# Kernel tuning notes

Hardware: AMD Instinct MI355X
Metric: run time of the kernel (lower is better)

Reference implementation:

```python
import jax, jax.numpy as jnp
import numpy as np


def setup_inputs() -> dict:
    key = jax.random.key(0)
    k1, k2 = jax.random.split(key)
    B, Lq, Lc, D = 16, 512, 2048, 1024
    question = jax.random.normal(k1, (B, Lq, D), dtype=jnp.float32)
    context = jax.random.normal(k2, (B, Lc, D), dtype=jnp.float32)
    return {"question": question, "context": context}


def reference(question, context):
    # e = context @ question^T : [B, Lc, Lq]  (unscaled)
    e = jnp.einsum("bcd,bqd->bcq", context, question)
    attn = jax.nn.softmax(e, axis=-1)
    # attention_output = attn @ question : [B, Lc, D]
    attn_out = jnp.einsum("bcq,bqd->bcd", attn, question)
    # concat along feature dim -> [B, Lc, 2D]; dropout is identity at eval
    return jnp.concatenate([context, attn_out], axis=-1)
```

## Files before the change

kernel.cpp:

```cpp
#include <hip/hip_runtime.h>

#define GAS __attribute__((address_space(1)))
#define LAS __attribute__((address_space(3)))

typedef __attribute__((ext_vector_type(8))) _Float16 half8;
typedef __attribute__((ext_vector_type(4))) float floatx4;
typedef __attribute__((ext_vector_type(4))) unsigned short ushort4v;

static constexpr int B_  = 16;
static constexpr int LQ  = 512;
static constexpr int LC  = 2048;
static constexpr int D_  = 1024;
static constexpr int DO  = 2048;
static constexpr int MT  = 64;

__device__ __forceinline__ void gl2lds16(const void* g, void* l) {
  __builtin_amdgcn_global_load_lds((const GAS unsigned int*)g,
                                   (LAS unsigned int*)l, 16, 0, 0);
}

__device__ __forceinline__ unsigned short f2h(float f) {
  return __builtin_bit_cast(unsigned short, (_Float16)f);
}

__global__ void conv_kernel(const float* __restrict__ src,
                            unsigned short* __restrict__ dst, int n4) {
  int i = blockIdx.x * blockDim.x + threadIdx.x;
  const int stride = gridDim.x * blockDim.x;
  for (; i < n4; i += stride) {
    const float4 v = ((const float4*)src)[i];
    ushort4v h;
    h.x = f2h(v.x); h.y = f2h(v.y); h.z = f2h(v.z); h.w = f2h(v.w);
    ((ushort4v*)dst)[i] = h;
  }
}

__global__ void qtransh_kernel(const unsigned short* __restrict__ qh,
                               unsigned short* __restrict__ qt) {
  __shared__ unsigned short t[32][33];
  const int b = blockIdx.z, d0 = blockIdx.x * 32, q0 = blockIdx.y * 32;
  const unsigned short* src = qh + (size_t)b * LQ * D_;
  unsigned short* dst = qt + (size_t)b * D_ * LQ;
  for (int i = threadIdx.y; i < 32; i += 8)
    t[i][threadIdx.x] = src[(size_t)(q0 + i) * D_ + d0 + threadIdx.x];
  __syncthreads();
  for (int i = threadIdx.y; i < 32; i += 8)
    dst[(size_t)(d0 + i) * LQ + q0 + threadIdx.x] = t[threadIdx.x][i];
}

__launch_bounds__(512, 4)
__global__ void attn_main(const unsigned short* __restrict__ qg,
                          const unsigned short* __restrict__ cg,
                          const unsigned short* __restrict__ qtg,
                          unsigned short* __restrict__ pg,
                          const float* __restrict__ cf,
                          float* __restrict__ og) {
  __shared__ __align__(16) char smem[32 * 1024 + 4 * 1024 + 2048 + 256];
  char* Qbuf = smem;
  char* Cbuf = smem + 32768;
  float* redf    = (float*)(smem + 36864);
  float* rowstat = (float*)(smem + 38912);

  const int tid  = threadIdx.x;
  const int wave = tid >> 6;
  const int lane = tid & 63;
  const int l15  = lane & 15;
  const int quad = lane >> 4;
  const int q8   = quad * 8;

  const int b    = blockIdx.x & 15;
  const int tile = blockIdx.x >> 4;
  const int c0   = tile * MT;

  const unsigned short* Q  = qg  + (size_t)b * LQ * D_;
  const unsigned short* C  = cg  + (size_t)b * LC * D_;
  const unsigned short* QT = qtg + (size_t)b * D_ * LQ;
  unsigned short*       P  = pg  + (size_t)b * LC * LQ;
  const float*          CF = cf  + (size_t)b * LC * D_;
  float*                O  = og  + (size_t)b * LC * DO;

  for (int i = tid; i < MT * (D_ / 4); i += 512) {
    const int r = i >> 8, ch = i & 255;
    ((float4*)(O + (size_t)(c0 + r) * DO))[ch] =
        ((const float4*)(CF + (size_t)(c0 + r) * D_))[ch];
  }

  floatx4 acc[4][4];
#pragma unroll
  for (int i = 0; i < 4; ++i)
#pragma unroll
    for (int j = 0; j < 4; ++j) acc[i][j] = floatx4{0.f, 0.f, 0.f, 0.f};

#pragma unroll 1
  for (int it = 0; it < 32; ++it) {
    const int k0 = it * 32;
#pragma unroll
    for (int j = 0; j < 5; ++j) {
      const int bb = wave + j * 8;
      if (bb < 36) {
        const unsigned short* g;
        char* l;
        if (bb < 32) {
          g = Q + (size_t)(bb * 16 + l15) * D_ + k0 + q8;
          l = Qbuf + bb * 1024;
        } else {
          const int mt = bb - 32;
          g = C + (size_t)(c0 + mt * 16 + l15) * D_ + k0 + q8;
          l = Cbuf + mt * 1024;
        }
        gl2lds16(g, l);
      }
    }
    __syncthreads();
    half8 af[4], bf[4];
#pragma unroll
    for (int mt = 0; mt < 4; ++mt)
      af[mt] = *(const half8*)(Cbuf + mt * 1024 + lane * 16);
#pragma unroll
    for (int nt = 0; nt < 4; ++nt)
      bf[nt] = *(const half8*)(Qbuf + (wave * 4 + nt) * 1024 + lane * 16);
#pragma unroll
    for (int mt = 0; mt < 4; ++mt)
#pragma unroll
      for (int nt = 0; nt < 4; ++nt)
        acc[mt][nt] = __builtin_amdgcn_mfma_f32_16x16x32_f16(
            af[mt], bf[nt], acc[mt][nt], 0, 0, 0);
    __syncthreads();
  }

#pragma unroll
  for (int mt = 0; mt < 4; ++mt)
#pragma unroll
    for (int r = 0; r < 4; ++r) {
      float m = fmaxf(fmaxf(acc[mt][0][r], acc[mt][1][r]),
                      fmaxf(acc[mt][2][r], acc[mt][3][r]));
      m = fmaxf(m, __shfl_xor(m, 1, 64));
      m = fmaxf(m, __shfl_xor(m, 2, 64));
      m = fmaxf(m, __shfl_xor(m, 4, 64));
      m = fmaxf(m, __shfl_xor(m, 8, 64));
      if (l15 == 0) redf[wave * 64 + mt * 16 + quad * 4 + r] = m;
    }
  __syncthreads();
  if (tid < 64) {
    float m = redf[tid];
#pragma unroll
    for (int w = 1; w < 8; ++w) m = fmaxf(m, redf[w * 64 + tid]);
    rowstat[tid] = m;
  }
  __syncthreads();
#pragma unroll
  for (int mt = 0; mt < 4; ++mt)
#pragma unroll
    for (int r = 0; r < 4; ++r) {
      const float m = rowstat[mt * 16 + quad * 4 + r];
      float s = 0.f;
#pragma unroll
      for (int nt = 0; nt < 4; ++nt) {
        const float e = __expf(acc[mt][nt][r] - m);
        acc[mt][nt][r] = e;
        s += e;
      }
      s += __shfl_xor(s, 1, 64);
      s += __shfl_xor(s, 2, 64);
      s += __shfl_xor(s, 4, 64);
      s += __shfl_xor(s, 8, 64);
      if (l15 == 0) redf[wave * 64 + mt * 16 + quad * 4 + r] = s;
    }
  __syncthreads();
  if (tid < 64) {
    float s = 0.f;
#pragma unroll
    for (int w = 0; w < 8; ++w) s += redf[w * 64 + tid];
    rowstat[tid] = 1.0f / s;
  }
  __syncthreads();
#pragma unroll
  for (int mt = 0; mt < 4; ++mt)
#pragma unroll
    for (int r = 0; r < 4; ++r) {
      const float inv = rowstat[mt * 16 + quad * 4 + r];
      const size_t rowoff =
          (size_t)(c0 + mt * 16 + quad * 4 + r) * LQ + wave * 64 + l15;
#pragma unroll
      for (int nt = 0; nt < 4; ++nt)
        P[rowoff + nt * 16] = f2h(acc[mt][nt][r] * inv);
    }
  __syncthreads();

#pragma unroll 1
  for (int nh = 0; nh < 2; ++nh) {
#pragma unroll
    for (int i = 0; i < 4; ++i)
#pragma unroll
      for (int j = 0; j < 4; ++j) acc[i][j] = floatx4{0.f, 0.f, 0.f, 0.f};
#pragma unroll 1
    for (int itq = 0; itq < 16; ++itq) {
      const int kq = itq * 32;
#pragma unroll
      for (int j = 0; j < 5; ++j) {
        const int bb = wave + j * 8;
        if (bb < 36) {
          const unsigned short* g;
          char* l;
          if (bb < 32) {
            g = QT + (size_t)(nh * 512 + bb * 16 + l15) * LQ + kq + q8;
            l = Qbuf + bb * 1024;
          } else {
            const int mt = bb - 32;
            g = P + (size_t)(c0 + mt * 16 + l15) * LQ + kq + q8;
            l = Cbuf + mt * 1024;
          }
          gl2lds16(g, l);
        }
      }
      __syncthreads();
      half8 af[4], bf[4];
#pragma unroll
      for (int mt = 0; mt < 4; ++mt)
        af[mt] = *(const half8*)(Cbuf + mt * 1024 + lane * 16);
#pragma unroll
      for (int nt = 0; nt < 4; ++nt)
        bf[nt] = *(const half8*)(Qbuf + (wave * 4 + nt) * 1024 + lane * 16);
#pragma unroll
      for (int mt = 0; mt < 4; ++mt)
#pragma unroll
        for (int nt = 0; nt < 4; ++nt)
          acc[mt][nt] = __builtin_amdgcn_mfma_f32_16x16x32_f16(
              af[mt], bf[nt], acc[mt][nt], 0, 0, 0);
      __syncthreads();
    }
#pragma unroll
    for (int mt = 0; mt < 4; ++mt)
#pragma unroll
      for (int r = 0; r < 4; ++r) {
        const size_t rowoff = (size_t)(c0 + mt * 16 + quad * 4 + r) * DO +
                              D_ + nh * 512 + wave * 64 + l15;
#pragma unroll
        for (int nt = 0; nt < 4; ++nt)
          O[rowoff + nt * 16] = acc[mt][nt][r];
      }
  }
}

extern "C" void kernel_launch(void* const* d_in, const int* in_sizes, int n_in,
                              void* d_out, int out_size, void* d_ws, size_t ws_size,
                              hipStream_t stream) {
  (void)in_sizes; (void)n_in; (void)out_size; (void)ws_size;
  const float* q = (const float*)d_in[0];
  const float* c = (const float*)d_in[1];
  float* out = (float*)d_out;
  unsigned short* qh  = (unsigned short*)d_ws;
  unsigned short* ch  = qh  + (size_t)B_ * LQ * D_;
  unsigned short* qth = ch  + (size_t)B_ * LC * D_;
  unsigned short* p   = qth + (size_t)B_ * D_ * LQ;
  conv_kernel<<<1024, 256, 0, stream>>>(q, qh, (B_ * LQ * D_) / 4);
  conv_kernel<<<2048, 256, 0, stream>>>(c, ch, (B_ * LC * D_) / 4);
  qtransh_kernel<<<dim3(D_ / 32, LQ / 32, B_), dim3(32, 8), 0, stream>>>(qh, qth);
  attn_main<<<dim3(B_ * (LC / MT)), dim3(512), 0, stream>>>(qh, ch, qth, p, c, out);
}
```

Before: 587.2 us.

## Double-buffer LDS tiles in both GEMM loops and fuse input prep kernels

Both GEMM phases of the main kernel now use two LDS buffers. The next k-slice is issued with global_load_lds before computing on the current one, with explicit vmcnt waits and raw s_barrier replacing the two __syncthreads per iteration. Q conversion and transpose are merged into one kernel, and the context fp32 copy into the output is moved from attn_main into the context conversion kernel, which cuts a launch and an extra pass over data. Doubling LDS to about 74KB per block may lower occupancy, and the hand-set vmcnt counts depend on how many loads each wave issues.

Result: faster. 567.0 us (-3.5%).

```diff
diff --git a/kernel.cpp b/kernel.cpp
--- a/kernel.cpp
+++ b/kernel.cpp
@@ -13,6 +13,7 @@
 static constexpr int D_  = 1024;
 static constexpr int DO  = 2048;
 static constexpr int MT  = 64;
+static constexpr int BUFSZ = 36864;
 
 __device__ __forceinline__ void gl2lds16(const void* g, void* l) {
   __builtin_amdgcn_global_load_lds((const GAS unsigned int*)g,
@@ -23,29 +24,35 @@
   return __builtin_bit_cast(unsigned short, (_Float16)f);
 }
 
-__global__ void conv_kernel(const float* __restrict__ src,
-                            unsigned short* __restrict__ dst, int n4) {
-  int i = blockIdx.x * blockDim.x + threadIdx.x;
-  const int stride = gridDim.x * blockDim.x;
-  for (; i < n4; i += stride) {
-    const float4 v = ((const float4*)src)[i];
+__global__ void qprep_kernel(const float* __restrict__ q,
+                             unsigned short* __restrict__ qh,
+                             unsigned short* __restrict__ qt) {
+  __shared__ unsigned short t[32][33];
+  const int b = blockIdx.z, d0 = blockIdx.x * 32, q0 = blockIdx.y * 32;
+  const float* src = q + (size_t)b * LQ * D_;
+  unsigned short* dq = qh + (size_t)b * LQ * D_;
+  unsigned short* dt = qt + (size_t)b * D_ * LQ;
+  for (int i = threadIdx.y; i < 32; i += 8) {
+    const unsigned short h = f2h(src[(size_t)(q0 + i) * D_ + d0 + threadIdx.x]);
+    dq[(size_t)(q0 + i) * D_ + d0 + threadIdx.x] = h;
+    t[i][threadIdx.x] = h;
+  }
+  __syncthreads();
+  for (int i = threadIdx.y; i < 32; i += 8)
+    dt[(size_t)(d0 + i) * LQ + q0 + threadIdx.x] = t[threadIdx.x][i];
+}
+
+__global__ void cprep_kernel(const float* __restrict__ src,
+                             unsigned short* __restrict__ dst,
+                             float* __restrict__ out) {
+  const int nrows = B_ * LC;
+  for (int row = blockIdx.x; row < nrows; row += gridDim.x) {
+    const float4 v = ((const float4*)(src + (size_t)row * D_))[threadIdx.x];
     ushort4v h;
     h.x = f2h(v.x); h.y = f2h(v.y); h.z = f2h(v.z); h.w = f2h(v.w);
-    ((ushort4v*)dst)[i] = h;
-  }
-}
-
-__global__ void qtransh_kernel(const unsigned short* __restrict__ qh,
-                               unsigned short* __restrict__ qt) {
-  __shared__ unsigned short t[32][33];
-  const int b = blockIdx.z, d0 = blockIdx.x * 32, q0 = blockIdx.y * 32;
-  const unsigned short* src = qh + (size_t)b * LQ * D_;
-  unsigned short* dst = qt + (size_t)b * D_ * LQ;
-  for (int i = threadIdx.y; i < 32; i += 8)
-    t[i][threadIdx.x] = src[(size_t)(q0 + i) * D_ + d0 + threadIdx.x];
-  __syncthreads();
-  for (int i = threadIdx.y; i < 32; i += 8)
-    dst[(size_t)(d0 + i) * LQ + q0 + threadIdx.x] = t[threadIdx.x][i];
+    ((ushort4v*)(dst + (size_t)row * D_))[threadIdx.x] = h;
+    ((float4*)(out + (size_t)row * DO))[threadIdx.x] = v;
+  }
 }
 
 __launch_bounds__(512, 4)
@@ -53,13 +60,10 @@
                           const unsigned short* __restrict__ cg,
                           const unsigned short* __restrict__ qtg,
                           unsigned short* __restrict__ pg,
-                          const float* __restrict__ cf,
                           float* __restrict__ og) {
-  __shared__ __align__(16) char smem[32 * 1024 + 4 * 1024 + 2048 + 256];
-  char* Qbuf = smem;
-  char* Cbuf = smem + 32768;
-  float* redf    = (float*)(smem + 36864);
-  float* rowstat = (float*)(smem + 38912);
+  __shared__ __align__(16) char smem[2 * BUFSZ + 2048 + 256];
+  float* redf    = (float*)(smem + 2 * BUFSZ);
+  float* rowstat = (float*)(smem + 2 * BUFSZ + 2048);
 
   const int tid  = threadIdx.x;
   const int wave = tid >> 6;
@@ -76,56 +80,83 @@
   const unsigned short* C  = cg  + (size_t)b * LC * D_;
   const unsigned short* QT = qtg + (size_t)b * D_ * LQ;
   unsigned short*       P  = pg  + (size_t)b * LC * LQ;
-  const float*          CF = cf  + (size_t)b * LC * D_;
   float*                O  = og  + (size_t)b * LC * DO;
 
-  for (int i = tid; i < MT * (D_ / 4); i += 512) {
-    const int r = i >> 8, ch = i & 255;
-    ((float4*)(O + (size_t)(c0 + r) * DO))[ch] =
-        ((const float4*)(CF + (size_t)(c0 + r) * D_))[ch];
-  }
-
   floatx4 acc[4][4];
-#pragma unroll
-  for (int i = 0; i < 4; ++i)
-#pragma unroll
-    for (int j = 0; j < 4; ++j) acc[i][j] = floatx4{0.f, 0.f, 0.f, 0.f};
-
-#pragma unroll 1
-  for (int it = 0; it < 32; ++it) {
+
+  auto stage1 = [&](int it, char* buf) {
     const int k0 = it * 32;
 #pragma unroll
     for (int j = 0; j < 5; ++j) {
       const int bb = wave + j * 8;
-      if (bb < 36) {
-        const unsigned short* g;
-        char* l;
-        if (bb < 32) {
-          g = Q + (size_t)(bb * 16 + l15) * D_ + k0 + q8;
-          l = Qbuf + bb * 1024;
-        } else {
-          const int mt = bb - 32;
-          g = C + (size_t)(c0 + mt * 16 + l15) * D_ + k0 + q8;
-          l = Cbuf + mt * 1024;
-        }
-        gl2lds16(g, l);
-      }
-    }
-    __syncthreads();
+      if (bb < 32) {
+        gl2lds16(Q + (size_t)(bb * 16 + l15) * D_ + k0 + q8, buf + bb * 1024);
+      } else if (bb < 36) {
+        const int mt = bb - 32;
+        gl2lds16(C + (size_t)(c0 + mt * 16 + l15) * D_ + k0 + q8,
+                 buf + 32768 + mt * 1024);
+      }
+    }
+  };
+
+  auto stage2 = [&](int nh, int itq, char* buf) {
+    const int kq = itq * 32;
+#pragma unroll
+    for (int j = 0; j < 5; ++j) {
+      const int bb = wave + j * 8;
+      if (bb < 32) {
+        gl2lds16(QT + (size_t)(nh * 512 + bb * 16 + l15) * LQ + kq + q8,
+                 buf + bb * 1024);
+      } else if (bb < 36) {
+        const int mt = bb - 32;
+        gl2lds16(P + (size_t)(c0 + mt * 16 + l15) * LQ + kq + q8,
+                 buf + 32768 + mt * 1024);
+      }
+    }
+  };
+
+  auto compute = [&](const char* buf) {
     half8 af[4], bf[4];
 #pragma unroll
     for (int mt = 0; mt < 4; ++mt)
-      af[mt] = *(const half8*)(Cbuf + mt * 1024 + lane * 16);
+      af[mt] = *(const half8*)(buf + 32768 + mt * 1024 + lane * 16);
 #pragma unroll
     for (int nt = 0; nt < 4; ++nt)
-      bf[nt] = *(const half8*)(Qbuf + (wave * 4 + nt) * 1024 + lane * 16);
+      bf[nt] = *(const half8*)(buf + (wave * 4 + nt) * 1024 + lane * 16);
 #pragma unroll
     for (int mt = 0; mt < 4; ++mt)
 #pragma unroll
       for (int nt = 0; nt < 4; ++nt)
         acc[mt][nt] = __builtin_amdgcn_mfma_f32_16x16x32_f16(
             af[mt], bf[nt], acc[mt][nt], 0, 0, 0);
-    __syncthreads();
+  };
+
+  auto wait_prev = [&]() {
+    if (wave < 4) asm volatile("s_waitcnt vmcnt(5)" ::: "memory");
+    else          asm volatile("s_waitcnt vmcnt(4)" ::: "memory");
+  };
+
+#pragma unroll
+  for (int i = 0; i < 4; ++i)
+#pragma unroll
+    for (int j = 0; j < 4; ++j) acc[i][j] = floatx4{0.f, 0.f, 0.f, 0.f};
+
+  stage1(0, smem);
+  int cur = 0;
+#pragma unroll 1
+  for (int it = 0; it < 32; ++it) {
+    if (it + 1 < 32) {
+      stage1(it + 1, smem + (cur ^ 1) * BUFSZ);
+      wait_prev();
+    } else {
+      asm volatile("s_waitcnt vmcnt(0)" ::: "memory");
+    }
+    __builtin_amdgcn_s_barrier();
+    __builtin_amdgcn_sched_barrier(0);
+    compute(smem + cur * BUFSZ);
+    asm volatile("" ::: "memory");
+    __builtin_amdgcn_s_barrier();
+    cur ^= 1;
   }
 
 #pragma unroll
@@ -185,6 +216,7 @@
       for (int nt = 0; nt < 4; ++nt)
         P[rowoff + nt * 16] = f2h(acc[mt][nt][r] * inv);
     }
+  asm volatile("s_waitcnt vmcnt(0)" ::: "memory");
   __syncthreads();
 
 #pragma unroll 1
@@ -193,41 +225,22 @@
     for (int i = 0; i < 4; ++i)
 #pragma unroll
       for (int j = 0; j < 4; ++j) acc[i][j] = floatx4{0.f, 0.f, 0.f, 0.f};
+    stage2(nh, 0, smem);
+    cur = 0;
 #pragma unroll 1
     for (int itq = 0; itq < 16; ++itq) {
-      const int kq = itq * 32;
-#pragma unroll
-      for (int j = 0; j < 5; ++j) {
-        const int bb = wave + j * 8;
-        if (bb < 36) {
-          const unsigned short* g;
-          char* l;
-          if (bb < 32) {
-            g = QT + (size_t)(nh * 512 + bb * 16 + l15) * LQ + kq + q8;
-            l = Qbuf + bb * 1024;
-          } else {
-            const int mt = bb - 32;
-            g = P + (size_t)(c0 + mt * 16 + l15) * LQ + kq + q8;
-            l = Cbuf + mt * 1024;
-          }
-          gl2lds16(g, l);
-        }
-      }
-      __syncthreads();
-      half8 af[4], bf[4];
-#pragma unroll
-      for (int mt = 0; mt < 4; ++mt)
-        af[mt] = *(const half8*)(Cbuf + mt * 1024 + lane * 16);
-#pragma unroll
-      for (int nt = 0; nt < 4; ++nt)
-        bf[nt] = *(const half8*)(Qbuf + (wave * 4 + nt) * 1024 + lane * 16);
-#pragma unroll
-      for (int mt = 0; mt < 4; ++mt)
-#pragma unroll
-        for (int nt = 0; nt < 4; ++nt)
-          acc[mt][nt] = __builtin_amdgcn_mfma_f32_16x16x32_f16(
-              af[mt], bf[nt], acc[mt][nt], 0, 0, 0);
-      __syncthreads();
+      if (itq + 1 < 16) {
+        stage2(nh, itq + 1, smem + (cur ^ 1) * BUFSZ);
+        wait_prev();
+      } else {
+        asm volatile("s_waitcnt vmcnt(0)" ::: "memory");
+      }
+      __builtin_amdgcn_s_barrier();
+      __builtin_amdgcn_sched_barrier(0);
+      compute(smem + cur * BUFSZ);
+      asm volatile("" ::: "memory");
+      __builtin_amdgcn_s_barrier();
+      cur ^= 1;
     }
 #pragma unroll
     for (int mt = 0; mt < 4; ++mt)
@@ -253,8 +266,7 @@
   unsigned short* ch  = qh  + (size_t)B_ * LQ * D_;
   unsigned short* qth = ch  + (size_t)B_ * LC * D_;
   unsigned short* p   = qth + (size_t)B_ * D_ * LQ;
-  conv_kernel<<<1024, 256, 0, stream>>>(q, qh, (B_ * LQ * D_) / 4);
-  conv_kernel<<<2048, 256, 0, stream>>>(c, ch, (B_ * LC * D_) / 4);
-  qtransh_kernel<<<dim3(D_ / 32, LQ / 32, B_), dim3(32, 8), 0, stream>>>(qh, qth);
-  attn_main<<<dim3(B_ * (LC / MT)), dim3(512), 0, stream>>>(qh, ch, qth, p, c, out);
-}
+  qprep_kernel<<<dim3(D_ / 32, LQ / 32, B_), dim3(32, 8), 0, stream>>>(q, qh, qth);
+  cprep_kernel<<<2048, 256, 0, stream>>>(c, ch, out);
+  attn_main<<<dim3(B_ * (LC / MT)), dim3(512), 0, stream>>>(qh, ch, qth, p, out);
+}
```
